# Performance work log

Hardware: AMD Instinct MI355X
Metric: run time of the kernel (lower is better)

## Reference

```python
import itertools
import jax, jax.numpy as jnp
import numpy as np

B, RES = 256, 16
DIM, KEY_DIM, NUM_HEADS, ATTN_RATIO = 448, 32, 8, 4
SEQ = RES * RES
EXP_KEY_DIM = ATTN_RATIO * KEY_DIM          # 128
TOTAL_KEY = KEY_DIM * NUM_HEADS             # 256
TOTAL_EXP = EXP_KEY_DIM * NUM_HEADS         # 1024
QKV_DIM = TOTAL_EXP + 2 * TOTAL_KEY         # 1536
SCALE = KEY_DIM ** -0.5


def _build_bias_idxs():
    # Replicates the itertools.product loop from build()
    points = list(itertools.product(range(RES), range(RES)))
    offsets = {}
    idxs = []
    for p1 in points:
        for p2 in points:
            off = (abs(p1[0] - p2[0]), abs(p1[1] - p2[1]))
            if off not in offsets:
                offsets[off] = len(offsets)
            idxs.append(offsets[off])
    return np.asarray(idxs, dtype=np.int32).reshape(SEQ, SEQ), len(offsets)


def setup_inputs() -> dict:
    key = jax.random.key(0)
    ks = jax.random.split(key, 6)
    bias_idxs_np, n_off = _build_bias_idxs()
    std = 0.02
    return {
        "hidden_states": jax.random.normal(ks[0], (B, SEQ, DIM), dtype=jnp.float32),
        "qkv_w": jax.random.normal(ks[1], (DIM, QKV_DIM), dtype=jnp.float32) * std,
        "qkv_b": jnp.zeros((QKV_DIM,), dtype=jnp.float32),
        "proj_w": jax.random.normal(ks[2], (TOTAL_EXP, DIM), dtype=jnp.float32) * std,
        "proj_b": jnp.zeros((DIM,), dtype=jnp.float32),
        "attention_biases": jax.random.normal(ks[3], (NUM_HEADS, n_off), dtype=jnp.float32) * std,
        "attention_bias_idxs": jnp.asarray(bias_idxs_np),
    }


def reference(hidden_states, qkv_w, qkv_b, proj_w, proj_b, attention_biases, attention_bias_idxs):
    b, s, _ = hidden_states.shape
    qkv = hidden_states @ qkv_w + qkv_b                       # [B,S,1536]
    qkv = qkv.reshape(b, s, NUM_HEADS, KEY_DIM * 2 + EXP_KEY_DIM)
    q, k, v = jnp.split(qkv, [KEY_DIM, 2 * KEY_DIM], axis=3)  # [B,S,H,dk],[B,S,H,dk],[B,S,H,dv]
    scores = jnp.einsum("bqhd,bkhd->bhqk", q, k) * SCALE      # [B,H,S,S]
    bias = attention_biases[:, attention_bias_idxs]           # [H,S,S] gather
    probs = jax.nn.softmax(scores + bias[None], axis=-1)
    ctx = jnp.einsum("bhqk,bkhd->bqhd", probs, v)             # [B,S,H,dv]
    ctx = ctx.reshape(b, s, TOTAL_EXP)
    return ctx @ proj_w + proj_b
```

## Files before the change

### kernel.cpp

```cpp
#include <hip/hip_runtime.h>
#include <hip/hip_bf16.h>
#include <stdint.h>


typedef __attribute__((ext_vector_type(4))) float f32x4;
typedef __attribute__((ext_vector_type(8))) short short8;
typedef __attribute__((ext_vector_type(4))) unsigned short u16x4;

#define DEVINL static __device__ __forceinline__

DEVINL unsigned short f2bf(float f) {
  unsigned u = __float_as_uint(f);
  return (unsigned short)((u + 0x7FFFu + ((u >> 16) & 1u)) >> 16);
}
DEVINL float bf2f(short s) {
  return __uint_as_float(((unsigned)(unsigned short)s) << 16);
}

DEVINL void gload_lds16(const void* g, void* l) {
  __builtin_amdgcn_global_load_lds((const __attribute__((address_space(1))) void*)g,
                                   (__attribute__((address_space(3))) void*)l,
                                   16, 0, 0);
}

#define SCALE 0.17677669529663687f

#define WS_XB     ((size_t)0)
#define WS_CTX    ((size_t)0)
#define WS_WQT    ((size_t)134217728)
#define WS_WPT    ((size_t)135593984)
#define WS_QW     ((size_t)136642560)
#define WS_KW     ((size_t)170196992)
#define WS_VT     ((size_t)203751424)
#define WS_QKVBP  ((size_t)342163456)

DEVINL int qkv_perm(int np, float* sc) {
  *sc = 1.0f;
  if (np < 512) {
    const int h = np >> 6, c = np & 63;
    if (c < 32) *sc = SCALE;
    return h * 192 + c;
  }
  const int h = (np - 512) >> 7, e = (np - 512) & 127;
  return h * 192 + 64 + e;
}


__global__ void k_convert_x(const float* __restrict__ x, short* __restrict__ xb) {
  const size_t i = (size_t)blockIdx.x * blockDim.x + threadIdx.x;
  const f32x4* src = (const f32x4*)x + i * 2;
  f32x4 a = src[0], b = src[1];
  short8 o;
#pragma unroll
  for (int t = 0; t < 4; ++t) o[t] = (short)f2bf(a[t]);
#pragma unroll
  for (int t = 0; t < 4; ++t) o[4 + t] = (short)f2bf(b[t]);
  ((short8*)xb)[i] = o;
}

__global__ void k_prep_qkvw(const float* __restrict__ w, short* __restrict__ out) {
  const int idx = blockIdx.x * blockDim.x + threadIdx.x;
  if (idx >= 1536 * 448) return;
  const int np = idx / 448, k = idx - np * 448;
  float sc;
  const int n = qkv_perm(np, &sc);
  out[idx] = (short)f2bf(w[(size_t)k * 1536 + n] * sc);
}

__global__ void k_prep_qkvb(const float* __restrict__ bsrc, float* __restrict__ bdst) {
  const int np = blockIdx.x * blockDim.x + threadIdx.x;
  if (np >= 1536) return;
  float sc;
  const int n = qkv_perm(np, &sc);
  bdst[np] = bsrc[n] * sc;
}

__global__ void k_transpose_bf16(const float* __restrict__ in, short* __restrict__ out,
                                 int K, int N, int total) {
  const int idx = blockIdx.x * blockDim.x + threadIdx.x;
  if (idx >= total) return;
  const int n = idx / K, k = idx - n * K;
  const float v = (n < N) ? in[(size_t)k * N + n] : 0.0f;
  out[idx] = (short)f2bf(v);
}


template <int KSTEPS, int LDA, int LDB>
DEVINL void gemm128_body(const short* __restrict__ A, const short* __restrict__ B,
                         short* Asm, short* Bsm, int m0, int n0, int tid,
                         f32x4 acc[4][4]) {
  const int lane = tid & 63, wave = tid >> 6;
  const int l15 = lane & 15, g = lane >> 4;
  const int wm = wave >> 1, wn = wave & 1;
  const int r8 = lane >> 3;
  const int scol = (((lane & 7) ^ r8) << 3);
  const int wbase = wave * 32;

  for (int ks = 0; ks < KSTEPS; ++ks) {
    const int k0 = ks * 64;
#pragma unroll
    for (int c = 0; c < 4; ++c) {
      const int br = wbase + c * 8;
      gload_lds16(A + (size_t)(m0 + br + r8) * LDA + k0 + scol, Asm + br * 64);
      gload_lds16(B + (size_t)(n0 + br + r8) * LDB + k0 + scol, Bsm + br * 64);
    }
    __syncthreads();
#pragma unroll
    for (int s = 0; s < 2; ++s) {
      const int rslot = (((s * 4 + g) ^ (l15 & 7)) << 3);
      short8 a[4], b[4];
#pragma unroll
      for (int i = 0; i < 4; ++i)
        a[i] = *(const short8*)(Asm + (wm * 64 + i * 16 + l15) * 64 + rslot);
#pragma unroll
      for (int j = 0; j < 4; ++j)
        b[j] = *(const short8*)(Bsm + (wn * 64 + j * 16 + l15) * 64 + rslot);
#pragma unroll
      for (int i = 0; i < 4; ++i)
#pragma unroll
        for (int j = 0; j < 4; ++j)
          acc[i][j] = __builtin_amdgcn_mfma_f32_16x16x32_bf16(a[i], b[j], acc[i][j], 0, 0, 0);
    }
    __syncthreads();
  }
}


union QkvSmem {
  struct { short a[128 * 64]; short b[128 * 64]; } ab;
  short tile[128 * 136];
};

__global__ __launch_bounds__(256) void k_qkv_gemm(
    const short* __restrict__ Xb, const short* __restrict__ Wt,
    const float* __restrict__ qkvbp,
    short* __restrict__ Qw, short* __restrict__ Kw, short* __restrict__ Vt) {
  __shared__ __align__(16) QkvSmem sm;
  const int tid = threadIdx.x;
  const int l = (blockIdx.x & 7) * 768 + (blockIdx.x >> 3);
  const int mt = l / 12, by = l - mt * 12;
  const int m0 = mt * 128, n0 = by * 128;
  f32x4 acc[4][4];
#pragma unroll
  for (int i = 0; i < 4; ++i)
#pragma unroll
    for (int j = 0; j < 4; ++j) acc[i][j] = (f32x4){0.f, 0.f, 0.f, 0.f};

  gemm128_body<7, 448, 448>(Xb, Wt, sm.ab.a, sm.ab.b, m0, n0, tid, acc);

  const int lane = tid & 63, wave = tid >> 6;
  const int l15 = lane & 15, g = lane >> 4;
  const int wm = wave >> 1, wn = wave & 1;
  const int b0 = m0 >> 8, s0 = m0 & 255;

  if (by >= 4) {
#pragma unroll
    for (int i = 0; i < 4; ++i) {
#pragma unroll
      for (int j = 0; j < 4; ++j) {
        const float bv = qkvbp[n0 + wn * 64 + j * 16 + l15];
        u16x4 pk;
#pragma unroll
        for (int r = 0; r < 4; ++r) pk[r] = f2bf(acc[i][j][r] + bv);
        *(u16x4*)&sm.tile[(wn * 64 + j * 16 + l15) * 136 + wm * 64 + i * 16 + g * 4] = pk;
      }
    }
    __syncthreads();
    const int bh = b0 * 8 + (by - 4);
#pragma unroll
    for (int p = 0; p < 8; ++p) {
      const int er = p * 16 + (tid >> 4);
      const int sc = (tid & 15) * 8;
      short8 v = *(const short8*)&sm.tile[er * 136 + sc];
      *(short8*)(Vt + (size_t)bh * 33792 + er * 264 + s0 + sc) = v;
    }
  } else {
#pragma unroll
    for (int i = 0; i < 4; ++i) {
#pragma unroll
      for (int j = 0; j < 4; ++j) {
        const float bv = qkvbp[n0 + wn * 64 + j * 16 + l15];
#pragma unroll
        for (int r = 0; r < 4; ++r)
          sm.tile[(wm * 64 + i * 16 + g * 4 + r) * 136 + wn * 64 + j * 16 + l15] =
              (short)f2bf(acc[i][j][r] + bv);
      }
    }
    __syncthreads();
    const int h0 = by * 2;
#pragma unroll
    for (int p = 0; p < 8; ++p) {
      const int row = p * 16 + (tid >> 4);
      const int ch = tid & 15;
      short8 v = *(const short8*)&sm.tile[row * 136 + ch * 8];
      const int hl = ch >> 3, cl = (ch & 7) * 8;
      const int bh = b0 * 8 + h0 + hl;
      short* dst = (cl < 32) ? (Qw + (size_t)bh * 8192 + (s0 + row) * 32 + cl)
                             : (Kw + (size_t)bh * 8192 + (s0 + row) * 32 + (cl - 32));
      *(short8*)dst = v;
    }
  }
}


__global__ __launch_bounds__(512, 4) void k_attn(
    const short* __restrict__ Qw, const short* __restrict__ Kw,
    const short* __restrict__ Vt, const float* __restrict__ attb, int n_off,
    short* __restrict__ CTX) {
  __shared__ short Ps[4][32 * 264];
  __shared__ float rinv[4][32];
  __shared__ float bias_sm[256];

  const int tid = threadIdx.x, lane = tid & 63, wave = tid >> 6;
  const int l15 = lane & 15, g = lane >> 4;
  const int bh = blockIdx.x;
  const int b = bh >> 3, h = bh & 7;

  if (tid < 256) bias_sm[tid] = attb[h * n_off + tid];
  __syncthreads();

  const short* Qb = Qw + (size_t)bh * 8192;
  const short* Kb = Kw + (size_t)bh * 8192;
  const short* Vb = Vt + (size_t)bh * 33792;

  for (int ph = 0; ph < 2; ++ph) {
    const int Q0 = ph * 128;

    {
      short8 aq[4][2];
#pragma unroll
      for (int u = 0; u < 4; ++u)
#pragma unroll
        for (int i = 0; i < 2; ++i)
          aq[u][i] = *(const short8*)(Qb + (Q0 + u * 32 + i * 16 + l15) * 32 + g * 8);

#pragma unroll
      for (int fj = 0; fj < 2; ++fj) {
        const int kk0 = wave * 32 + fj * 16;
        const short8 bk = *(const short8*)(Kb + (kk0 + l15) * 32 + g * 8);
        const int kk = kk0 + l15;
        const int kr = kk >> 4, kc = kk & 15;
#pragma unroll
        for (int u = 0; u < 4; ++u) {
#pragma unroll
          for (int i = 0; i < 2; ++i) {
            const int q0 = Q0 + u * 32 + i * 16;
            f32x4 acc;
#pragma unroll
            for (int r = 0; r < 4; ++r) {
              const int qrow = q0 + g * 4 + r;
              const int qr = qrow >> 4, qc = qrow & 15;
              const int a = (qr > kr) ? qr - kr : kr - qr;
              const int bo = (qc > kc) ? qc - kc : kc - qc;
              acc[r] = bias_sm[a * 16 + bo];
            }
            acc = __builtin_amdgcn_mfma_f32_16x16x32_bf16(aq[u][i], bk, acc, 0, 0, 0);
#pragma unroll
            for (int r = 0; r < 4; ++r)
              Ps[u][(i * 16 + g * 4 + r) * 264 + kk] = (short)f2bf(acc[r]);
          }
        }
      }
    }
    __syncthreads();

    {
      const int r = tid >> 4, part = tid & 15;
#pragma unroll
      for (int u = 0; u < 4; ++u) {
        short* rowp = &Ps[u][r * 264 + part * 16];
        short8 x0 = ((const short8*)rowp)[0];
        short8 x1 = ((const short8*)rowp)[1];
        float v[16];
#pragma unroll
        for (int t = 0; t < 8; ++t) { v[t] = bf2f(x0[t]); v[8 + t] = bf2f(x1[t]); }
        float mx = v[0];
#pragma unroll
        for (int t = 1; t < 16; ++t) mx = fmaxf(mx, v[t]);
#pragma unroll
        for (int d = 1; d < 16; d <<= 1) mx = fmaxf(mx, __shfl_xor(mx, d));
        float sum = 0.f;
#pragma unroll
        for (int t = 0; t < 16; ++t) { v[t] = __expf(v[t] - mx); sum += v[t]; }
#pragma unroll
        for (int d = 1; d < 16; d <<= 1) sum += __shfl_xor(sum, d);
        short8 o0, o1;
#pragma unroll
        for (int t = 0; t < 8; ++t) { o0[t] = (short)f2bf(v[t]); o1[t] = (short)f2bf(v[8 + t]); }
        ((short8*)rowp)[0] = o0;
        ((short8*)rowp)[1] = o1;
        if (part == 0) rinv[u][r] = 1.0f / sum;
      }
    }
    __syncthreads();

    {
      f32x4 cacc[4][2];
#pragma unroll
      for (int u = 0; u < 4; ++u)
#pragma unroll
        for (int qt = 0; qt < 2; ++qt) cacc[u][qt] = (f32x4){0.f, 0.f, 0.f, 0.f};

      const int e = wave * 16 + l15;
#pragma unroll
      for (int ks = 0; ks < 8; ++ks) {
        const short8 bv = *(const short8*)(Vb + e * 264 + ks * 32 + g * 8);
#pragma unroll
        for (int u = 0; u < 4; ++u)
#pragma unroll
          for (int qt = 0; qt < 2; ++qt) {
            const short8 ap = *(const short8*)&Ps[u][(qt * 16 + l15) * 264 + ks * 32 + g * 8];
            cacc[u][qt] = __builtin_amdgcn_mfma_f32_16x16x32_bf16(ap, bv, cacc[u][qt], 0, 0, 0);
          }
      }

#pragma unroll
      for (int u = 0; u < 4; ++u)
#pragma unroll
        for (int qt = 0; qt < 2; ++qt) {
          const int qb = qt * 16 + g * 4;
#pragma unroll
          for (int r = 0; r < 4; ++r) {
            const int q = Q0 + u * 32 + qb + r;
            CTX[((size_t)b * 256 + q) * 1024 + h * 128 + wave * 16 + l15] =
                (short)f2bf(cacc[u][qt][r] * rinv[u][qb + r]);
          }
        }
    }
    __syncthreads();
  }
}


__global__ __launch_bounds__(256) void k_proj_gemm(
    const short* __restrict__ CTX, const short* __restrict__ Wpt,
    const float* __restrict__ projb, float* __restrict__ out) {
  __shared__ __align__(16) short Asm[128 * 64];
  __shared__ __align__(16) short Bsm[128 * 64];
  const int tid = threadIdx.x;
  const int l = (blockIdx.x & 7) * 256 + (blockIdx.x >> 3);
  const int mt = l >> 2, nt = l & 3;
  const int m0 = mt * 128, n0 = nt * 128;
  f32x4 acc[4][4];
#pragma unroll
  for (int i = 0; i < 4; ++i)
#pragma unroll
    for (int j = 0; j < 4; ++j) acc[i][j] = (f32x4){0.f, 0.f, 0.f, 0.f};

  gemm128_body<16, 1024, 1024>(CTX, Wpt, Asm, Bsm, m0, n0, tid, acc);

  const int lane = tid & 63, wave = tid >> 6;
  const int l15 = lane & 15, g = lane >> 4;
  const int wm = wave >> 1, wn = wave & 1;
#pragma unroll
  for (int i = 0; i < 4; ++i) {
    const int mb = m0 + wm * 64 + i * 16 + g * 4;
#pragma unroll
    for (int j = 0; j < 4; ++j) {
      const int n = n0 + wn * 64 + j * 16 + l15;
      if (n < 448) {
        const float bv = projb[n];
#pragma unroll
        for (int r = 0; r < 4; ++r)
          out[(size_t)(mb + r) * 448 + n] = acc[i][j][r] + bv;
      }
    }
  }
}


extern "C" void kernel_launch(void* const* d_in, const int* in_sizes, int n_in,
                              void* d_out, int out_size, void* d_ws, size_t ws_size,
                              hipStream_t stream) {
  const float* X      = (const float*)d_in[0];
  const float* qkv_w  = (const float*)d_in[1];
  const float* qkv_b  = (const float*)d_in[2];
  const float* proj_w = (const float*)d_in[3];
  const float* proj_b = (const float*)d_in[4];
  const float* att_b  = (const float*)d_in[5];
  const int n_off = in_sizes[5] / 8;

  char* ws = (char*)d_ws;
  short* Xb    = (short*)(ws + WS_XB);
  short* CTX   = (short*)(ws + WS_CTX);
  short* WQT   = (short*)(ws + WS_WQT);
  short* WPT   = (short*)(ws + WS_WPT);
  short* Qw    = (short*)(ws + WS_QW);
  short* Kw    = (short*)(ws + WS_KW);
  short* Vt    = (short*)(ws + WS_VT);
  float* QKVBP = (float*)(ws + WS_QKVBP);

  k_convert_x<<<14336, 256, 0, stream>>>(X, Xb);
  k_prep_qkvw<<<(1536 * 448 + 255) / 256, 256, 0, stream>>>(qkv_w, WQT);
  k_prep_qkvb<<<6, 256, 0, stream>>>(qkv_b, QKVBP);
  k_transpose_bf16<<<(512 * 1024 + 255) / 256, 256, 0, stream>>>(proj_w, WPT, 1024, 448, 512 * 1024);

  k_qkv_gemm<<<6144, 256, 0, stream>>>(Xb, WQT, QKVBP, Qw, Kw, Vt);
  k_attn<<<2048, 512, 0, stream>>>(Qw, Kw, Vt, att_b, n_off, CTX);
  k_proj_gemm<<<2048, 256, 0, stream>>>(CTX, WPT, proj_b, (float*)d_out);
}
```

Measured before the change: 415.3 us.

## Double-buffer LDS in GEMM mainloop and write Q/K directly via swapped MFMA

```diff
diff --git a/kernel.cpp b/kernel.cpp
--- a/kernel.cpp
+++ b/kernel.cpp
@@ -85,8 +85,8 @@
 }
 
 
-template <int KSTEPS, int LDA, int LDB>
-DEVINL void gemm128_body(const short* __restrict__ A, const short* __restrict__ B,
+template <int KSTEPS, int LDA, int LDB, bool SWAP>
+DEVINL void gemm128_pipe(const short* __restrict__ A, const short* __restrict__ B,
                          short* Asm, short* Bsm, int m0, int n0, int tid,
                          f32x4 acc[4][4]) {
   const int lane = tid & 63, wave = tid >> 6;
@@ -96,30 +96,43 @@
   const int scol = (((lane & 7) ^ r8) << 3);
   const int wbase = wave * 32;
 
+  const short* Ab = A + (size_t)(m0 + wbase + r8) * LDA + scol;
+  const short* Bb = B + (size_t)(n0 + wbase + r8) * LDB + scol;
+
+#pragma unroll
+  for (int c = 0; c < 4; ++c) {
+    gload_lds16(Ab + (size_t)(c * 8) * LDA, Asm + (wbase + c * 8) * 64);
+    gload_lds16(Bb + (size_t)(c * 8) * LDB, Bsm + (wbase + c * 8) * 64);
+  }
+  __syncthreads();
+
   for (int ks = 0; ks < KSTEPS; ++ks) {
-    const int k0 = ks * 64;
-#pragma unroll
-    for (int c = 0; c < 4; ++c) {
-      const int br = wbase + c * 8;
-      gload_lds16(A + (size_t)(m0 + br + r8) * LDA + k0 + scol, Asm + br * 64);
-      gload_lds16(B + (size_t)(n0 + br + r8) * LDB + k0 + scol, Bsm + br * 64);
-    }
-    __syncthreads();
+    const int cur = ks & 1, nxt = cur ^ 1;
+    if (ks + 1 < KSTEPS) {
+      const int k0 = (ks + 1) * 64;
+#pragma unroll
+      for (int c = 0; c < 4; ++c) {
+        gload_lds16(Ab + (size_t)(c * 8) * LDA + k0, Asm + nxt * 8192 + (wbase + c * 8) * 64);
+        gload_lds16(Bb + (size_t)(c * 8) * LDB + k0, Bsm + nxt * 8192 + (wbase + c * 8) * 64);
+      }
+    }
 #pragma unroll
     for (int s = 0; s < 2; ++s) {
       const int rslot = (((s * 4 + g) ^ (l15 & 7)) << 3);
       short8 a[4], b[4];
 #pragma unroll
       for (int i = 0; i < 4; ++i)
-        a[i] = *(const short8*)(Asm + (wm * 64 + i * 16 + l15) * 64 + rslot);
+        a[i] = *(const short8*)(Asm + cur * 8192 + (wm * 64 + i * 16 + l15) * 64 + rslot);
 #pragma unroll
       for (int j = 0; j < 4; ++j)
-        b[j] = *(const short8*)(Bsm + (wn * 64 + j * 16 + l15) * 64 + rslot);
+        b[j] = *(const short8*)(Bsm + cur * 8192 + (wn * 64 + j * 16 + l15) * 64 + rslot);
 #pragma unroll
       for (int i = 0; i < 4; ++i)
 #pragma unroll
         for (int j = 0; j < 4; ++j)
-          acc[i][j] = __builtin_amdgcn_mfma_f32_16x16x32_bf16(a[i], b[j], acc[i][j], 0, 0, 0);
+          acc[i][j] = SWAP
+              ? __builtin_amdgcn_mfma_f32_16x16x32_bf16(b[j], a[i], acc[i][j], 0, 0, 0)
+              : __builtin_amdgcn_mfma_f32_16x16x32_bf16(a[i], b[j], acc[i][j], 0, 0, 0);
     }
     __syncthreads();
   }
@@ -127,7 +140,7 @@
 
 
 union QkvSmem {
-  struct { short a[128 * 64]; short b[128 * 64]; } ab;
+  struct { short a[2 * 8192]; short b[2 * 8192]; } ab;
   short tile[128 * 136];
 };
 
@@ -140,20 +153,20 @@
   const int l = (blockIdx.x & 7) * 768 + (blockIdx.x >> 3);
   const int mt = l / 12, by = l - mt * 12;
   const int m0 = mt * 128, n0 = by * 128;
-  f32x4 acc[4][4];
-#pragma unroll
-  for (int i = 0; i < 4; ++i)
-#pragma unroll
-    for (int j = 0; j < 4; ++j) acc[i][j] = (f32x4){0.f, 0.f, 0.f, 0.f};
-
-  gemm128_body<7, 448, 448>(Xb, Wt, sm.ab.a, sm.ab.b, m0, n0, tid, acc);
 
   const int lane = tid & 63, wave = tid >> 6;
   const int l15 = lane & 15, g = lane >> 4;
   const int wm = wave >> 1, wn = wave & 1;
   const int b0 = m0 >> 8, s0 = m0 & 255;
 
+  f32x4 acc[4][4];
+#pragma unroll
+  for (int i = 0; i < 4; ++i)
+#pragma unroll
+    for (int j = 0; j < 4; ++j) acc[i][j] = (f32x4){0.f, 0.f, 0.f, 0.f};
+
   if (by >= 4) {
+    gemm128_pipe<7, 448, 448, false>(Xb, Wt, sm.ab.a, sm.ab.b, m0, n0, tid, acc);
 #pragma unroll
     for (int i = 0; i < 4; ++i) {
 #pragma unroll
@@ -175,29 +188,24 @@
       *(short8*)(Vt + (size_t)bh * 33792 + er * 264 + s0 + sc) = v;
     }
   } else {
+    gemm128_pipe<7, 448, 448, true>(Xb, Wt, sm.ab.a, sm.ab.b, m0, n0, tid, acc);
 #pragma unroll
     for (int i = 0; i < 4; ++i) {
+      const int s = s0 + wm * 64 + i * 16 + l15;
 #pragma unroll
       for (int j = 0; j < 4; ++j) {
-        const float bv = qkvbp[n0 + wn * 64 + j * 16 + l15];
-#pragma unroll
-        for (int r = 0; r < 4; ++r)
-          sm.tile[(wm * 64 + i * 16 + g * 4 + r) * 136 + wn * 64 + j * 16 + l15] =
-              (short)f2bf(acc[i][j][r] + bv);
-      }
-    }
-    __syncthreads();
-    const int h0 = by * 2;
-#pragma unroll
-    for (int p = 0; p < 8; ++p) {
-      const int row = p * 16 + (tid >> 4);
-      const int ch = tid & 15;
-      short8 v = *(const short8*)&sm.tile[row * 136 + ch * 8];
-      const int hl = ch >> 3, cl = (ch & 7) * 8;
-      const int bh = b0 * 8 + h0 + hl;
-      short* dst = (cl < 32) ? (Qw + (size_t)bh * 8192 + (s0 + row) * 32 + cl)
-                             : (Kw + (size_t)bh * 8192 + (s0 + row) * 32 + (cl - 32));
-      *(short8*)dst = v;
+        const int nbase = n0 + wn * 64 + j * 16 + g * 4;
+        const f32x4 bv4 = *(const f32x4*)(qkvbp + nbase);
+        u16x4 pk;
+#pragma unroll
+        for (int r = 0; r < 4; ++r) pk[r] = f2bf(acc[i][j][r] + bv4[r]);
+        const int h = (nbase >> 6) & 7, c = nbase & 63;
+        const int bh = b0 * 8 + (by << 1) + (nbase >> 6 & 1);
+        short* dst = (c < 32) ? (Qw + ((size_t)bh * 256 + s) * 32 + c)
+                              : (Kw + ((size_t)bh * 256 + s) * 32 + (c - 32));
+        *(u16x4*)dst = pk;
+        (void)h;
+      }
     }
   }
 }
@@ -335,8 +343,8 @@
 __global__ __launch_bounds__(256) void k_proj_gemm(
     const short* __restrict__ CTX, const short* __restrict__ Wpt,
     const float* __restrict__ projb, float* __restrict__ out) {
-  __shared__ __align__(16) short Asm[128 * 64];
-  __shared__ __align__(16) short Bsm[128 * 64];
+  __shared__ __align__(16) short Asm[2 * 8192];
+  __shared__ __align__(16) short Bsm[2 * 8192];
   const int tid = threadIdx.x;
   const int l = (blockIdx.x & 7) * 256 + (blockIdx.x >> 3);
   const int mt = l >> 2, nt = l & 3;
@@ -347,7 +355,7 @@
 #pragma unroll
     for (int j = 0; j < 4; ++j) acc[i][j] = (f32x4){0.f, 0.f, 0.f, 0.f};
 
-  gemm128_body<16, 1024, 1024>(CTX, Wpt, Asm, Bsm, m0, n0, tid, acc);
+  gemm128_pipe<16, 1024, 1024, false>(CTX, Wpt, Asm, Bsm, m0, n0, tid, acc);
 
   const int lane = tid & 63, wave = tid >> 6;
   const int l15 = lane & 15, g = lane >> 4;
```

Result: faster. 391.7 us (-5.7%).
